# Kernel tuning notes

Hardware: AMD Instinct MI355X
Metric: run time of the kernel (lower is better)

The kernel has to match this reference:

```python
import jax, jax.numpy as jnp
from jax import lax
import numpy as np

H = 48; W = 48; C_IN = 256; A_PER = 3
M = A_PER * H * W            # 6912 anchors
IMG = 768.0                  # square image, clip bound for x and y
OBJ_THR = 0.3; IOU_THR = 0.7; TOP_K = 2000
NEG = -1e9                   # finite sentinel for masked scores


def _make_anchors():
    stride = IMG / H
    base = 2.0 * stride
    ratios = np.array([0.5, 1.0, 2.0])
    ws = base * np.sqrt(ratios)          # [3]
    hs = base / np.sqrt(ratios)
    cx = (np.arange(W) + 0.5) * stride
    cy = (np.arange(H) + 0.5) * stride
    cxg, cyg = np.meshgrid(cx, cy)       # [H, W]
    anc = np.stack([
        cxg[None] - ws[:, None, None] / 2,
        cyg[None] - hs[:, None, None] / 2,
        cxg[None] + ws[:, None, None] / 2,
        cyg[None] + hs[:, None, None] / 2,
    ], axis=-1)                           # [3, H, W, 4] matches (anchor, h, w) flatten order
    return jnp.asarray(anc.reshape(-1, 4), jnp.float32)


def setup_inputs() -> dict:
    key = jax.random.key(0)
    ks = jax.random.split(key, 4)
    x = jax.random.normal(ks[0], (1, C_IN, H, W), jnp.float32)
    conv_w = jax.random.normal(ks[1], (256, 256, 3, 3), jnp.float32) * 0.02
    conv_b = jnp.zeros((256,), jnp.float32)
    det_w = jax.random.normal(ks[2], (3, 256, 1, 1), jnp.float32) * 0.02
    det_b = jnp.zeros((3,), jnp.float32)
    reg_w = jax.random.normal(ks[3], (12, 256, 1, 1), jnp.float32) * 0.02
    reg_b = jnp.zeros((12,), jnp.float32)
    anchors = _make_anchors()
    return {"x": x, "conv_w": conv_w, "conv_b": conv_b, "det_w": det_w,
            "det_b": det_b, "reg_w": reg_w, "reg_b": reg_b, "anchors": anchors}


def reference(x, conv_w, conv_b, det_w, det_b, reg_w, reg_b, anchors):
    # ---- FPN 3x3 conv + RPN head (1x1 convs) ----
    inter = lax.conv_general_dilated(
        x, conv_w, (1, 1), 'SAME',
        dimension_numbers=('NCHW', 'OIHW', 'NCHW')) + conv_b[None, :, None, None]
    obj = jax.nn.sigmoid(jnp.einsum('nchw,oc->nohw', inter, det_w[:, :, 0, 0])
                         + det_b[None, :, None, None])          # [1,3,H,W]
    reg = (jnp.einsum('nchw,oc->nohw', inter, reg_w[:, :, 0, 0])
           + reg_b[None, :, None, None])                        # [1,12,H,W]

    scores = obj.reshape(-1)                                    # [M], (anchor,h,w) order
    deltas = reg.reshape(1, 4, A_PER, H, W).transpose(0, 2, 3, 4, 1).reshape(-1, 4)

    # ---- box decode (preserves the source's cx/cy quirk: cx = y1 + w/2, cy = x1 + h/2) ----
    x1, y1, x2, y2 = anchors[:, 0], anchors[:, 1], anchors[:, 2], anchors[:, 3]
    aw = x2 - x1; ah = y2 - y1
    acx = y1 + aw / 2; acy = x1 + ah / 2
    dx, dy, dw, dh = deltas[:, 0], deltas[:, 1], deltas[:, 2], deltas[:, 3]
    px = acx + dx * aw; py = acy + dy * ah
    pw = aw * jnp.exp(dw); ph = ah * jnp.exp(dh)
    boxes = jnp.stack([px - pw / 2, py - ph / 2, px + pw / 2, py + ph / 2], axis=-1)

    # ---- clip to image ----
    boxes = jnp.clip(boxes, 0.0, IMG)

    # ---- validity: degenerate filter (source's naming quirk) + objectness threshold ----
    hts = boxes[:, 2] - boxes[:, 0]
    wds = boxes[:, 3] - boxes[:, 1]
    valid = (hts > 0) & (wds > 0) & (scores > OBJ_THR)

    # ---- greedy NMS (jit-friendly: sort, pairwise IoU, sequential suppression) ----
    s = jnp.where(valid, scores, NEG)
    order = jnp.argsort(-s)
    b = boxes[order]; v = valid[order]; ss = s[order]
    area = (b[:, 2] - b[:, 0]) * (b[:, 3] - b[:, 1])             # [M]
    iw = jnp.clip(jnp.minimum(b[:, None, 2], b[None, :, 2])
                  - jnp.maximum(b[:, None, 0], b[None, :, 0]), 0.0)
    ih = jnp.clip(jnp.minimum(b[:, None, 3], b[None, :, 3])
                  - jnp.maximum(b[:, None, 1], b[None, :, 1]), 0.0)
    inter_a = iw * ih                                             # [M,M]
    iou = inter_a / jnp.maximum(area[:, None] + area[None, :] - inter_a, 1e-9)

    idx = jnp.arange(M)

    def body(suppressed, i):
        keep_i = v[i] & (~suppressed[i])
        sup = keep_i & (iou[i] > IOU_THR) & (idx > i)
        return suppressed | sup, keep_i

    _, keeps = lax.scan(body, jnp.zeros(M, bool), idx)            # keep mask (sorted order)

    # ---- top-k proposal selection (fixed K, padded with sentinels) ----
    out_s = jnp.where(keeps, ss, NEG)
    topv, topi = lax.top_k(out_s, TOP_K)
    vtop = keeps[topi]
    out_scores = jnp.where(vtop, topv, -1.0)                      # [TOP_K]
    out_boxes = jnp.where(vtop[:, None], b[topi], 0.0)            # [TOP_K, 4]
    return out_scores, out_boxes
```

## Files before the change

### kernel.cpp

```cpp
#include <hip/hip_runtime.h>
#include <cstdint>

#define NPX 2304
#define MM 6912
#define NW 108
#define TOPK 2000
#define NEGV -1000000000.0f
#define OBJ_THRF 0.3f
#define IOU_THRF 0.7f
#define IMGF 768.0f
#define KSPLIT 8

typedef unsigned long long u64;
typedef unsigned int u32;
typedef unsigned short u16;

__device__ __forceinline__ u64 shfl64(u64 v, int src) {
  int lo = __shfl((int)(v & 0xffffffffull), src, 64);
  int hi = __shfl((int)(v >> 32), src, 64);
  return ((u64)(u32)hi << 32) | (u32)lo;
}

__global__ __launch_bounds__(256) void k_wt(const float* __restrict__ cw,
                                            float* __restrict__ wt) {
  __shared__ float t[64][65];
  const int it0 = blockIdx.x * 64;
  const int oc0 = blockIdx.y * 64;
  const int tx = threadIdx.x & 63;
  const int ty = threadIdx.x >> 6;
#pragma unroll
  for (int k = 0; k < 16; ++k) {
    int oc = ty + k * 4;
    t[oc][tx] = cw[(oc0 + oc) * 2304 + it0 + tx];
  }
  __syncthreads();
#pragma unroll
  for (int k = 0; k < 16; ++k) {
    int it = ty + k * 4;
    wt[(it0 + it) * 256 + oc0 + tx] = t[tx][it];
  }
}

__global__ __launch_bounds__(256) void k_conv(const float* __restrict__ x,
                                              const float* __restrict__ wt,
                                              float* __restrict__ part) {
  __shared__ float xs[16 * 8 * 52];
  const int tid = threadIdx.x;
  const int px = blockIdx.x * 256 + tid;
  const int oc0 = blockIdx.y * 16;
  const int ks = blockIdx.z;
  const int row = px / 48, col = px % 48;
  const int r0 = (blockIdx.x * 256) / 48;
  const int rbase = row - r0;

  float acc[16];
#pragma unroll
  for (int k = 0; k < 16; ++k) acc[k] = 0.f;

  for (int icc = 0; icc < 2; ++icc) {
    const int ic0 = ks * 32 + icc * 16;
    for (int e = tid; e < 16 * 8 * 50; e += 256) {
      int ic = e / 400, rem = e % 400;
      int r = rem / 50, c = rem % 50 - 1;
      int gr = r0 - 1 + r;
      float v = 0.f;
      if (c >= 0 && c < 48 && gr >= 0 && gr < 48)
        v = x[(ic0 + ic) * NPX + gr * 48 + c];
      xs[(ic * 8 + r) * 52 + (c + 1)] = v;
    }
    __syncthreads();
    for (int ic = 0; ic < 16; ++ic) {
      float xv[9];
#pragma unroll
      for (int dr = 0; dr < 3; ++dr)
#pragma unroll
        for (int dc = 0; dc < 3; ++dc)
          xv[dr * 3 + dc] = xs[(ic * 8 + rbase + dr) * 52 + col + dc];
      const float* wrow = wt + (size_t)(ic0 + ic) * 9 * 256 + oc0;
#pragma unroll
      for (int t = 0; t < 9; ++t) {
        const float* wp = wrow + t * 256;
#pragma unroll
        for (int k = 0; k < 16; ++k) acc[k] += xv[t] * wp[k];
      }
    }
    __syncthreads();
  }
#pragma unroll
  for (int k = 0; k < 16; ++k)
    part[((size_t)ks * 256 + oc0 + k) * NPX + px] = acc[k];
}

__global__ __launch_bounds__(256) void k_decode(const float* __restrict__ part,
                                                const float* __restrict__ cb,
                                                const float* __restrict__ dw,
                                                const float* __restrict__ db,
                                                const float* __restrict__ rw,
                                                const float* __restrict__ rb,
                                                const float* __restrict__ anch,
                                                float* __restrict__ s,
                                                float4* __restrict__ boxes) {
  __shared__ float wl[256 * 16];
  __shared__ float red[4 * 64 * 17];
  const int tid = threadIdx.x;
  const int pxl = tid & 63;
  const int cq = tid >> 6;
  const int px = blockIdx.x * 64 + pxl;
  for (int e = tid; e < 3840; e += 256) {
    int o = e % 15, c = e / 15;
    wl[c * 16 + o] = (o < 3) ? dw[o * 256 + c] : rw[(o - 3) * 256 + c];
  }
  __syncthreads();
  float acc[15];
#pragma unroll
  for (int o = 0; o < 15; o++) acc[o] = 0.f;
  for (int ci = 0; ci < 64; ++ci) {
    int c = cq * 64 + ci;
    float v = cb[c];
#pragma unroll
    for (int kks = 0; kks < KSPLIT; ++kks)
      v += part[((size_t)kks * 256 + c) * NPX + px];
#pragma unroll
    for (int o = 0; o < 15; o++) acc[o] += v * wl[c * 16 + o];
  }
#pragma unroll
  for (int o = 0; o < 15; o++) red[(cq * 64 + pxl) * 17 + o] = acc[o];
  __syncthreads();
  if (tid < 64) {
    const int p = blockIdx.x * 64 + tid;
    float a[15];
#pragma unroll
    for (int o = 0; o < 15; o++)
      a[o] = red[tid * 17 + o] + red[(64 + tid) * 17 + o] +
             red[(128 + tid) * 17 + o] + red[(192 + tid) * 17 + o];
    const float4* an4 = (const float4*)anch;
#pragma unroll
    for (int aa = 0; aa < 3; ++aa) {
      int m = aa * NPX + p;
      float logit = a[aa] + db[aa];
      float score = 1.f / (1.f + expf(-logit));
      float dxv = a[3 + 0 + aa] + rb[0 + aa];
      float dyv = a[3 + 3 + aa] + rb[3 + aa];
      float dwv = a[3 + 6 + aa] + rb[6 + aa];
      float dhv = a[3 + 9 + aa] + rb[9 + aa];
      float4 an = an4[m];
      float aw = an.z - an.x;
      float ah = an.w - an.y;
      float acx = an.y + aw * 0.5f;
      float acy = an.x + ah * 0.5f;
      float pxc = acx + dxv * aw;
      float pyc = acy + dyv * ah;
      float pw = aw * expf(dwv);
      float ph = ah * expf(dhv);
      float b0 = pxc - pw * 0.5f, b1 = pyc - ph * 0.5f;
      float b2 = pxc + pw * 0.5f, b3 = pyc + ph * 0.5f;
      b0 = fminf(fmaxf(b0, 0.f), IMGF);
      b1 = fminf(fmaxf(b1, 0.f), IMGF);
      b2 = fminf(fmaxf(b2, 0.f), IMGF);
      b3 = fminf(fmaxf(b3, 0.f), IMGF);
      float hts = b2 - b0, wds = b3 - b1;
      bool valid = (hts > 0.f) && (wds > 0.f) && (score > OBJ_THRF);
      s[m] = valid ? score : NEGV;
      boxes[m] = make_float4(b0, b1, b2, b3);
    }
  }
}

__global__ __launch_bounds__(256) void k_sortA(const float* __restrict__ s,
                                               u64* __restrict__ keys,
                                               u64* __restrict__ nz) {
  __shared__ u64 lds[1024];
  const int tid = threadIdx.x;
  const int b = blockIdx.x;
  for (int i = b * 256 + tid; i < MM * 2; i += 8 * 256) nz[i] = 0;
  for (int v = tid; v < 1024; v += 256) {
    int i = b * 1024 + v;
    u64 p;
    if (i < MM) {
      u32 u = __float_as_uint(s[i]);
      u = u ^ (u32)(((int)u >> 31) | 0x80000000);
      p = ((u64)(~u) << 32) | (u32)i;
    } else {
      p = ~0ull;
    }
    lds[v] = p;
  }
  for (u32 kk = 2; kk <= 1024; kk <<= 1) {
    for (u32 j = kk >> 1; j > 0; j >>= 1) {
      __syncthreads();
#pragma unroll 2
      for (int t = tid; t < 512; t += 256) {
        int i = ((t & ~(j - 1)) << 1) | (t & (j - 1));
        int l = i | j;
        bool up = ((i & kk) == 0);
        u64 a = lds[i], c = lds[l];
        u64 mn = a < c ? a : c;
        u64 mx = a < c ? c : a;
        lds[i] = up ? mn : mx;
        lds[l] = up ? mx : mn;
      }
    }
  }
  __syncthreads();
  for (int v = tid; v < 1024; v += 256) keys[b * 1024 + v] = lds[v];
}

__global__ __launch_bounds__(256) void k_merge(const u64* __restrict__ in,
                                               u64* __restrict__ outk, int L, int fin,
                                               const float* __restrict__ s,
                                               const float4* __restrict__ boxes,
                                               float* __restrict__ ssc,
                                               float4* __restrict__ sboxes) {
  const int i = blockIdx.x * 256 + threadIdx.x;
  const int pair = i / (2 * L);
  const int r = i - pair * 2 * L;
  const u64* A = in + (size_t)pair * 2 * L;
  const u64* B = A + L;
  int lo = (r > L) ? (r - L) : 0;
  int hi = (r < L) ? r : L;
  while (lo < hi) {
    int mid = (lo + hi) >> 1;
    if (A[mid] < B[r - 1 - mid]) lo = mid + 1; else hi = mid;
  }
  int a = lo, bi = r - lo;
  u64 av = (a < L) ? A[a] : ~0ull;
  u64 bv = (bi < L) ? B[bi] : ~0ull;
  u64 o = (av < bv) ? av : bv;
  outk[i] = o;
  if (fin && i < MM) {
    int idx = (int)(u32)o;
    ssc[i] = s[idx];
    sboxes[i] = boxes[idx];
  }
}

__global__ __launch_bounds__(256) void k_mask(const float4* __restrict__ sboxes,
                                              u64* __restrict__ mask_t,
                                              u64* __restrict__ nz) {
  __shared__ float4 rb_[64];
  const int rt = blockIdx.x;
  const int w = blockIdx.y * 4 + (threadIdx.x >> 6);
  const int lane = threadIdx.x & 63;
  if (threadIdx.x < 64) rb_[threadIdx.x] = sboxes[rt * 64 + threadIdx.x];
  __syncthreads();
  if (w < rt) return;
  float4 c = sboxes[w * 64 + lane];
  float areaC = (c.z - c.x) * (c.w - c.y);
  u64 myw = 0;
  for (int r = 0; r < 64; ++r) {
    float4 b = rb_[r];
    float iw = fmaxf(fminf(b.z, c.z) - fmaxf(b.x, c.x), 0.f);
    float ih = fmaxf(fminf(b.w, c.w) - fmaxf(b.y, c.y), 0.f);
    float inter = iw * ih;
    float areaB = (b.z - b.x) * (b.w - b.y);
    float un = fmaxf(areaB + areaC - inter, 1e-9f);
    bool bit = (inter / un) > IOU_THRF;
    u64 bal = __ballot(bit);
    if (lane == r) myw = bal;
  }
  mask_t[(size_t)w * MM + rt * 64 + lane] = myw;
  if (myw) atomicOr(&nz[(rt * 64 + lane) * 2 + (w >> 6)], 1ull << (w & 63));
}

__global__ __launch_bounds__(256) void k_scan(const u64* __restrict__ mask_t,
                                              const u64* __restrict__ nz,
                                              const float* __restrict__ ssc,
                                              const float4* __restrict__ sboxes,
                                              float* __restrict__ out) {
  __shared__ u64 diagL[NW * 64];
  __shared__ float sscL[MM];
  __shared__ u16 pairs[MM];
  __shared__ u64 nzTmp[128];
  __shared__ u64 remv[NW];
  __shared__ u64 keepw[NW];
  __shared__ int blist[64];
  __shared__ int nkS;
  __shared__ int kcntS;
  __shared__ int TS;
  __shared__ int pref[NW];
  const int tid = threadIdx.x;
  for (int e = tid; e < NW * 64; e += 256)
    diagL[e] = mask_t[(size_t)(e >> 6) * MM + (e >> 6) * 64 + (e & 63)];
  for (int e = tid; e < MM; e += 256) sscL[e] = ssc[e];
  if (tid < NW) { remv[tid] = 0; keepw[tid] = 0; }
  if (tid == 0) kcntS = 0;
  __syncthreads();

  for (int c = 0; c < NW; ++c) {
    if (tid >= 128) nzTmp[tid - 128] = nz[c * 128 + (tid - 128)];
    if (tid < 64) {
      const int lane = tid;
      u64 dg = diagL[c * 64 + lane];
      float sv = sscL[c * 64 + lane];
      u64 vb = __ballot(sv > OBJ_THRF);
      u64 w0 = remv[c];
      u64 cand = vb & ~w0;
      u64 above = (lane < 63) ? ~((2ull << lane) - 1ull) : 0ull;
      bool inC = ((cand >> lane) & 1ull) != 0;
      u64 conf = __ballot(inC && ((dg & above & cand) != 0ull));
      u64 kb;
      if (conf == 0ull) {
        kb = cand;
      } else {
        u64 w = w0;
        kb = 0;
        u64 rem = cand;
        while (rem) {
          int b = __ffsll(rem) - 1;
          kb |= (1ull << b);
          w |= shfl64(dg, b);
          rem = vb & ~w;
        }
      }
      int below = __popcll(kb & ((1ull << lane) - 1ull));
      if ((kb >> lane) & 1ull) blist[below] = lane;
      if (lane == 0) {
        keepw[c] = kb;
        nkS = __popcll(kb);
        kcntS += __popcll(kb);
      }
    }
    __syncthreads();
    const int nk = nkS;
    if (tid < 64) {
      u64 n0 = 0, n1 = 0;
      int b = 0;
      if (tid < nk) {
        b = blist[tid];
        n0 = nzTmp[2 * b];
        n1 = nzTmp[2 * b + 1];
        if (c < 64) {
          n0 &= (c < 63) ? ~((2ull << c) - 1ull) : 0ull;
        } else {
          n0 = 0;
          n1 &= ~((2ull << (c - 64)) - 1ull);
        }
      }
      int cnt = __popcll(n0) + __popcll(n1);
      int sc = cnt;
#pragma unroll
      for (int d = 1; d < 64; d <<= 1) {
        int o = __shfl_up(sc, d, 64);
        if (tid >= d) sc += o;
      }
      int base = sc - cnt;
      if (tid == 63) TS = sc;
      int k = 0;
      while (n0) {
        int wv = __ffsll(n0) - 1; n0 &= n0 - 1;
        pairs[base + k] = (u16)((wv << 6) | b); ++k;
      }
      while (n1) {
        int wv = __ffsll(n1) - 1; n1 &= n1 - 1;
        pairs[base + k] = (u16)(((wv + 64) << 6) | b); ++k;
      }
    }
    __syncthreads();
    const int T = TS;
    for (int p = tid; p < T; p += 256) {
      u32 pr = pairs[p];
      int wv = pr >> 6, b = pr & 63;
      u64 v = mask_t[(size_t)wv * MM + c * 64 + b];
      atomicOr(&remv[wv], v);
    }
    __syncthreads();
    if (kcntS >= TOPK) break;
  }

  if (tid == 0) {
    int run = 0;
    for (int cc = 0; cc < NW; ++cc) { pref[cc] = run; run += __popcll(keepw[cc]); }
  }
  __syncthreads();
  for (int e = tid; e < TOPK * 5; e += 256) out[e] = (e < TOPK) ? -1.0f : 0.0f;
  __syncthreads();
  float4* ob = (float4*)(out + TOPK);
  for (int i = tid; i < MM; i += 256) {
    int cc = i >> 6, b = i & 63;
    u64 kb = keepw[cc];
    if ((kb >> b) & 1ull) {
      int rank = pref[cc] + __popcll(kb & ((1ull << b) - 1ull));
      if (rank < TOPK) {
        out[rank] = sscL[i];
        ob[rank] = sboxes[i];
      }
    }
  }
}

extern "C" void kernel_launch(void* const* d_in, const int* in_sizes, int n_in,
                              void* d_out, int out_size, void* d_ws, size_t ws_size,
                              hipStream_t stream) {
  const float* x  = (const float*)d_in[0];
  const float* cw = (const float*)d_in[1];
  const float* cb = (const float*)d_in[2];
  const float* dw = (const float*)d_in[3];
  const float* db = (const float*)d_in[4];
  const float* rw = (const float*)d_in[5];
  const float* rb = (const float*)d_in[6];
  const float* an = (const float*)d_in[7];
  char* ws = (char*)d_ws;
  float*  part   = (float*)(ws);
  u64*    keysA  = (u64*)(ws);
  u64*    keysB  = (u64*)(ws + 65536);
  u64*    mask   = (u64*)(ws);
  u64*    nz     = (u64*)(ws + 5971968);
  float*  wt     = (float*)(ws + 18874368);
  float*  s      = (float*)(ws + 21233664);
  float4* boxes  = (float4*)(ws + 21261312);
  float*  ssc    = (float*)(ws + 21371904);
  float4* sboxes = (float4*)(ws + 21399552);
  float* out = (float*)d_out;

  hipLaunchKernelGGL(k_wt, dim3(36, 4), dim3(256), 0, stream, cw, wt);
  hipLaunchKernelGGL(k_conv, dim3(9, 16, KSPLIT), dim3(256), 0, stream, x, wt, part);
  hipLaunchKernelGGL(k_decode, dim3(36), dim3(256), 0, stream, part, cb, dw, db, rw, rb, an, s, boxes);
  hipLaunchKernelGGL(k_sortA, dim3(8), dim3(256), 0, stream, s, keysA, nz);
  hipLaunchKernelGGL(k_merge, dim3(32), dim3(256), 0, stream, keysA, keysB, 1024, 0, s, boxes, ssc, sboxes);
  hipLaunchKernelGGL(k_merge, dim3(32), dim3(256), 0, stream, keysB, keysA, 2048, 0, s, boxes, ssc, sboxes);
  hipLaunchKernelGGL(k_merge, dim3(32), dim3(256), 0, stream, keysA, keysB, 4096, 1, s, boxes, ssc, sboxes);
  hipLaunchKernelGGL(k_mask, dim3(108, 27), dim3(256), 0, stream, sboxes, mask, nz);
  hipLaunchKernelGGL(k_scan, dim3(1), dim3(256), 0, stream, mask, nz, ssc, sboxes, out);
}
```

Baseline: 270.1 us.

## Prefetch mask column slices into LDS in NMS scan and merge sort stages

```diff
diff --git a/kernel.cpp b/kernel.cpp
--- a/kernel.cpp
+++ b/kernel.cpp
@@ -10,6 +10,7 @@
 #define IOU_THRF 0.7f
 #define IMGF 768.0f
 #define KSPLIT 8
+#define SLW (NW * 64)
 
 typedef unsigned long long u64;
 typedef unsigned int u32;
@@ -166,15 +167,15 @@
   }
 }
 
-__global__ __launch_bounds__(256) void k_sortA(const float* __restrict__ s,
-                                               u64* __restrict__ keys,
-                                               u64* __restrict__ nz) {
-  __shared__ u64 lds[1024];
+__global__ __launch_bounds__(1024) void k_sortB(const float* __restrict__ s,
+                                                u64* __restrict__ keys,
+                                                u64* __restrict__ nz) {
+  __shared__ u64 lds[4096];
   const int tid = threadIdx.x;
   const int b = blockIdx.x;
-  for (int i = b * 256 + tid; i < MM * 2; i += 8 * 256) nz[i] = 0;
-  for (int v = tid; v < 1024; v += 256) {
-    int i = b * 1024 + v;
+  for (int i = b * 1024 + tid; i < MM * 2; i += 2048) nz[i] = 0;
+  for (int v = tid; v < 4096; v += 1024) {
+    int i = b * 4096 + v;
     u64 p;
     if (i < MM) {
       u32 u = __float_as_uint(s[i]);
@@ -185,11 +186,11 @@
     }
     lds[v] = p;
   }
-  for (u32 kk = 2; kk <= 1024; kk <<= 1) {
+  for (u32 kk = 2; kk <= 4096; kk <<= 1) {
     for (u32 j = kk >> 1; j > 0; j >>= 1) {
       __syncthreads();
 #pragma unroll 2
-      for (int t = tid; t < 512; t += 256) {
+      for (int t = tid; t < 2048; t += 1024) {
         int i = ((t & ~(j - 1)) << 1) | (t & (j - 1));
         int l = i | j;
         bool up = ((i & kk) == 0);
@@ -202,7 +203,7 @@
     }
   }
   __syncthreads();
-  for (int v = tid; v < 1024; v += 256) keys[b * 1024 + v] = lds[v];
+  for (int v = tid; v < 4096; v += 1024) keys[b * 4096 + v] = lds[v];
 }
 
 __global__ __launch_bounds__(256) void k_merge(const u64* __restrict__ in,
@@ -267,10 +268,10 @@
                                               const float* __restrict__ ssc,
                                               const float4* __restrict__ sboxes,
                                               float* __restrict__ out) {
-  __shared__ u64 diagL[NW * 64];
+  __shared__ u64 sliceL[2][SLW];
   __shared__ float sscL[MM];
-  __shared__ u16 pairs[MM];
-  __shared__ u64 nzTmp[128];
+  __shared__ u16 pairs[SLW];
+  __shared__ u64 nzT[128];
   __shared__ u64 remv[NW];
   __shared__ u64 keepw[NW];
   __shared__ int blist[64];
@@ -279,18 +280,28 @@
   __shared__ int TS;
   __shared__ int pref[NW];
   const int tid = threadIdx.x;
-  for (int e = tid; e < NW * 64; e += 256)
-    diagL[e] = mask_t[(size_t)(e >> 6) * MM + (e >> 6) * 64 + (e & 63)];
+  for (int e = tid; e < SLW; e += 256)
+    sliceL[0][e] = mask_t[(size_t)(e >> 6) * MM + (e & 63)];
   for (int e = tid; e < MM; e += 256) sscL[e] = ssc[e];
   if (tid < NW) { remv[tid] = 0; keepw[tid] = 0; }
   if (tid == 0) kcntS = 0;
   __syncthreads();
 
+  int cur = 0;
   for (int c = 0; c < NW; ++c) {
-    if (tid >= 128) nzTmp[tid - 128] = nz[c * 128 + (tid - 128)];
+    const u64* sl = sliceL[cur];
+    u64* np = sliceL[cur ^ 1];
+    if (tid >= 192) {
+      int j = tid - 192;
+      nzT[j] = nz[c * 128 + j];
+      nzT[j + 64] = nz[c * 128 + 64 + j];
+    } else if (tid >= 64 && c + 1 < NW) {
+      for (int e = tid - 64; e < 3456; e += 128)
+        np[e] = mask_t[(size_t)(e >> 6) * MM + (c + 1) * 64 + (e & 63)];
+    }
     if (tid < 64) {
       const int lane = tid;
-      u64 dg = diagL[c * 64 + lane];
+      u64 dg = sl[c * 64 + lane];
       float sv = sscL[c * 64 + lane];
       u64 vb = __ballot(sv > OBJ_THRF);
       u64 w0 = remv[c];
@@ -321,14 +332,18 @@
       }
     }
     __syncthreads();
+    if (tid >= 64 && tid < 192 && c + 1 < NW) {
+      for (int e = 3456 + (tid - 64); e < SLW; e += 128)
+        np[e] = mask_t[(size_t)(e >> 6) * MM + (c + 1) * 64 + (e & 63)];
+    }
     const int nk = nkS;
     if (tid < 64) {
       u64 n0 = 0, n1 = 0;
       int b = 0;
       if (tid < nk) {
         b = blist[tid];
-        n0 = nzTmp[2 * b];
-        n1 = nzTmp[2 * b + 1];
+        n0 = nzT[2 * b];
+        n1 = nzT[2 * b + 1];
         if (c < 64) {
           n0 &= (c < 63) ? ~((2ull << c) - 1ull) : 0ull;
         } else {
@@ -359,11 +374,11 @@
     const int T = TS;
     for (int p = tid; p < T; p += 256) {
       u32 pr = pairs[p];
-      int wv = pr >> 6, b = pr & 63;
-      u64 v = mask_t[(size_t)wv * MM + c * 64 + b];
-      atomicOr(&remv[wv], v);
+      int wv = pr >> 6, bb = pr & 63;
+      atomicOr(&remv[wv], sl[wv * 64 + bb]);
     }
     __syncthreads();
+    cur ^= 1;
     if (kcntS >= TOPK) break;
   }
 
@@ -415,9 +430,7 @@
   hipLaunchKernelGGL(k_wt, dim3(36, 4), dim3(256), 0, stream, cw, wt);
   hipLaunchKernelGGL(k_conv, dim3(9, 16, KSPLIT), dim3(256), 0, stream, x, wt, part);
   hipLaunchKernelGGL(k_decode, dim3(36), dim3(256), 0, stream, part, cb, dw, db, rw, rb, an, s, boxes);
-  hipLaunchKernelGGL(k_sortA, dim3(8), dim3(256), 0, stream, s, keysA, nz);
-  hipLaunchKernelGGL(k_merge, dim3(32), dim3(256), 0, stream, keysA, keysB, 1024, 0, s, boxes, ssc, sboxes);
-  hipLaunchKernelGGL(k_merge, dim3(32), dim3(256), 0, stream, keysB, keysA, 2048, 0, s, boxes, ssc, sboxes);
+  hipLaunchKernelGGL(k_sortB, dim3(2), dim3(1024), 0, stream, s, keysA, nz);
   hipLaunchKernelGGL(k_merge, dim3(32), dim3(256), 0, stream, keysA, keysB, 4096, 1, s, boxes, ssc, sboxes);
   hipLaunchKernelGGL(k_mask, dim3(108, 27), dim3(256), 0, stream, sboxes, mask, nz);
   hipLaunchKernelGGL(k_scan, dim3(1), dim3(256), 0, stream, mask, nz, ssc, sboxes, out);
```

After: 714.0 us. +164.4%, slower.
